# Kernel optimization log

Hardware: AMD Instinct MI355X
Metric: run time of the kernel (lower is better)

Reference implementation:

```python
import jax, jax.numpy as jnp
import numpy as np

B, CIN, COUT = 8, 16, 16
N_IN, N_OUT, E = 16384, 16384, 300000
FILTER_DIMS = [2, 16, 16, 16, 16, 16, CIN * COUT]  # spatial_dim -> filter_seq -> cin*cout


def setup_inputs() -> dict:
    key = jax.random.key(0)
    ks = jax.random.split(key, 12)
    points_in = jax.random.uniform(ks[0], (N_IN, 2), dtype=jnp.float32)
    points_out = jax.random.uniform(ks[1], (N_OUT, 2), dtype=jnp.float32)
    weights = jax.random.uniform(ks[2], (N_IN,), dtype=jnp.float32)  # quadrature weights
    features = jax.random.normal(ks[3], (B, CIN, N_IN), dtype=jnp.float32)
    idx_out = jnp.sort(jax.random.randint(ks[4], (E,), 0, N_OUT))
    idx_in = jax.random.randint(ks[5], (E,), 0, N_IN)
    eval_indices = jnp.stack([idx_out, idx_in], axis=1).astype(jnp.int32)
    inp = dict(points_in=points_in, points_out=points_out, weights=weights,
               features=features, eval_indices=eval_indices)
    for i in range(6):
        fan_in = FILTER_DIMS[i]
        inp[f"W{i}"] = (jax.random.normal(ks[6 + i], (FILTER_DIMS[i], FILTER_DIMS[i + 1]),
                                          dtype=jnp.float32) / np.float32(np.sqrt(fan_in)))
    return inp


def reference(points_in, points_out, weights, features, eval_indices, W0, W1, W2, W3, W4, W5):
    idx_out = eval_indices[:, 0]
    idx_in = eval_indices[:, 1]
    # eval_locs: [E, spatial_dim]
    locs = points_out[idx_out] - points_in[idx_in]
    # filter MLP with Sin activations, no bias (filter_mode='single')
    h = locs
    for W in (W0, W1, W2, W3, W4):
        h = jnp.sin(h @ W)
    filt = (h @ W5).reshape(-1, CIN, COUT)  # [E, cin, cout]
    w_e = weights[idx_in]                    # [E]
    feat_e = features[:, :, idx_in]          # [B, cin, E]
    # torch.einsum('n,nij,bin->bjn') -> per-edge values, laid out [E, B, cout] for segment_sum
    vals = jnp.einsum('e,eio,bie->ebo', w_e, filt, feat_e)
    integral = jax.ops.segment_sum(vals, idx_out, num_segments=N_OUT)  # [N_out, B, cout]
    return jnp.transpose(integral, (1, 2, 0))  # [B, cout, N_out]
```

## Files before the change

### kernel.cpp

```cpp
#include <hip/hip_runtime.h>

#define N_IN   16384
#define N_OUT  16384
#define NE     300000
#define SEGS   8
#define NWIN   (N_OUT / SEGS)
#define GRID_G 768
#define BKG    136
#define BSTR   544
#define SROW   256
#define NCHK   9375

#define MLPB   586
#define TRB    1024
#define SETB   80

typedef unsigned int   u32;
typedef unsigned short u16;
typedef __attribute__((ext_vector_type(4))) float f32x4;
typedef __attribute__((ext_vector_type(8))) short bf16x8;

__device__ __forceinline__ u16 f2bf(float x) {
    union { float f; u32 u; } v; v.f = x;
    u32 r = v.u + 0x7fffu + ((v.u >> 16) & 1u);
    return (u16)(r >> 16);
}

__device__ __forceinline__ float fast_sin(float t) {
    float r;
    asm("v_sin_f32 %0, %1" : "=v"(r) : "v"(t * 0.15915494309189535f));
    return r;
}

__global__ __launch_bounds__(256) void k_front(
        const float* __restrict__ pin, const float* __restrict__ pout,
        const float* __restrict__ wts, const int* __restrict__ ei,
        const float* __restrict__ W0, const float* __restrict__ W1,
        const float* __restrict__ W2, const float* __restrict__ W3,
        const float* __restrict__ W4, const float* __restrict__ W5,
        const float* __restrict__ feat,
        u16* __restrict__ ftb, u16* __restrict__ hB,
        int* __restrict__ segoff, u16* __restrict__ Bfrag) {
    __shared__ float tile[32][33];
    int tid = threadIdx.x, bid = blockIdx.x;

    if (bid < MLPB) {
        int e0 = (bid * 256 + tid) * 2;
        if (e0 >= NE) return;
        int4 q = *(const int4*)(ei + e0 * 2);
        float2 po0 = ((const float2*)pout)[q.x];
        float2 pi0 = ((const float2*)pin)[q.y];
        float2 po1 = ((const float2*)pout)[q.z];
        float2 pi1 = ((const float2*)pin)[q.w];
        float x0 = po0.x - pi0.x, y0 = po0.y - pi0.y;
        float x1 = po1.x - pi1.x, y1 = po1.y - pi1.y;

        float h0[16], h1[16];
#pragma unroll
        for (int j = 0; j < 16; ++j) {
            float wa = W0[j], wb = W0[16 + j];
            h0[j] = fast_sin(x0 * wa + y0 * wb);
            h1[j] = fast_sin(x1 * wa + y1 * wb);
        }
#pragma unroll
        for (int L = 0; L < 4; ++L) {
            const float* W = (L == 0) ? W1 : (L == 1) ? W2 : (L == 2) ? W3 : W4;
            float n0[16], n1[16];
#pragma unroll
            for (int j = 0; j < 16; ++j) {
                float a0 = 0.f, a1 = 0.f;
#pragma unroll
                for (int i = 0; i < 16; ++i) {
                    float w = W[i * 16 + j];
                    a0 = fmaf(h0[i], w, a0);
                    a1 = fmaf(h1[i], w, a1);
                }
                n0[j] = fast_sin(a0); n1[j] = fast_sin(a1);
            }
#pragma unroll
            for (int j = 0; j < 16; ++j) { h0[j] = n0[j]; h1[j] = n1[j]; }
        }
        float we0 = wts[q.y], we1 = wts[q.w];
        u16* hp = hB + ((size_t)(e0 >> 5)) * 512 + (e0 & 31);
#pragma unroll
        for (int j = 0; j < 16; ++j) {
            u32 pk = (u32)f2bf(we0 * h0[j]) | ((u32)f2bf(we1 * h1[j]) << 16);
            *(u32*)(hp + j * 32) = pk;
        }
    } else if (bid < MLPB + TRB) {
        int jb = (bid - MLPB) * 2;
        int tx = tid & 31, ty = tid >> 5;
#pragma unroll
        for (int t = 0; t < 2; ++t) {
            int job = jb + t;
            int n0 = (job & 511) * 32, c0 = (job >> 9) * 32;
#pragma unroll
            for (int k = 0; k < 4; ++k)
                tile[ty + k * 8][tx] = feat[(size_t)(c0 + ty + k * 8) * N_IN + n0 + tx];
            __syncthreads();
#pragma unroll
            for (int k = 0; k < 4; ++k)
                ftb[(size_t)(n0 + ty + k * 8) * 128 + c0 + tx] = f2bf(tile[tx][ty + k * 8]);
            __syncthreads();
        }
    } else {
        int g = (bid - MLPB - TRB) * 256 + tid;
        if (g <= N_OUT) {
            if (g == N_OUT) segoff[g] = NE;
            else {
                int lo = 0, hi = NE;
                while (lo < hi) { int m = (lo + hi) >> 1; if (ei[2 * m] < g) lo = m + 1; else hi = m; }
                segoff[g] = lo;
            }
        }
        if (g < 4096) {
            int ks = g >> 9, rem = g & 511, l = rem >> 3, e = rem & 7;
            int k = ks * 32 + ((l >> 4) << 3) + e;
            int o = l & 15;
            Bfrag[g] = f2bf(W5[(k >> 4) * 256 + ((k & 15) << 4) + o]);
        }
    }
}

#define EIW(IA, IB, BSE) do {                                             \
    int g_ = (BSE) + 2 * pr; g_ = g_ <= NE - 2 ? g_ : NE - 2;             \
    int4 q_ = *(const int4*)(ei + 2 * g_); IA = q_.y; IB = q_.w; } while (0)

#define FTW(FA, FB, IA, IB) do {                                          \
    FA = ftb4[(size_t)(u32)(IA) * 16 + oct];                              \
    FB = ftb4[(size_t)(u32)(IB) * 16 + oct]; } while (0)

#define BQW(BQ, BSE) do {                                                 \
    int ch_ = (BSE) >> 5; ch_ = ch_ <= NCHK - 1 ? ch_ : NCHK - 1;         \
    BQ = *(const bf16x8*)(hB + (size_t)ch_ * 512 + (j << 5) + (kg << 3)); } while (0)

#define STGW(DST, FA, FB) do {                                            \
    u32 aw_[4] = {FA.x, FA.y, FA.z, FA.w};                                \
    u32 bw_[4] = {FB.x, FB.y, FB.z, FB.w};                                \
    int wb_ = bloc * BSTR + (pr >> 2) * BKG + 2 * (pr & 3);               \
    _Pragma("unroll")                                                     \
    for (int m_ = 0; m_ < 8; ++m_) {                                      \
        u32 lo_ = (m_ & 1) ? (aw_[m_ >> 1] >> 16) : (aw_[m_ >> 1] & 0xffffu);      \
        u32 hi_ = (m_ & 1) ? (bw_[m_ >> 1] & 0xffff0000u) : (bw_[m_ >> 1] << 16);  \
        *(u32*)&(DST)[wb_ + (ibase + m_) * 8] = lo_ | hi_;                \
    } } while (0)

#define PIECE(KLO, KHI) do {                                              \
    if ((KLO) == 0 && (KHI) == 32) {                                      \
        acc0 = __builtin_amdgcn_mfma_f32_16x16x32_bf16(a0, bqC, acc0, 0, 0, 0); \
        acc1 = __builtin_amdgcn_mfma_f32_16x16x32_bf16(a1, bqC, acc1, 0, 0, 0); \
    } else {                                                              \
        bf16x8 bm_;                                                       \
        _Pragma("unroll")                                                 \
        for (int e_ = 0; e_ < 8; ++e_) {                                  \
            int k_ = kg * 8 + e_;                                         \
            bm_[e_] = (k_ >= (KLO) && k_ < (KHI)) ? bqC[e_] : (short)0;   \
        }                                                                 \
        acc0 = __builtin_amdgcn_mfma_f32_16x16x32_bf16(a0, bm_, acc0, 0, 0, 0); \
        acc1 = __builtin_amdgcn_mfma_f32_16x16x32_bf16(a1, bm_, acc1, 0, 0, 0); \
    } } while (0)

#define DUMP(SS) do {                                                     \
    u32 l0_ = (u32)f2bf(acc0[0]) | ((u32)f2bf(acc0[1]) << 16);            \
    u32 l1_ = (u32)f2bf(acc0[2]) | ((u32)f2bf(acc0[3]) << 16);            \
    *(uint2*)&S_lds[(b0 * SEGS + (SS)) * SROW + j * 16 + kg * 4] = make_uint2(l0_, l1_); \
    u32 l2_ = (u32)f2bf(acc1[0]) | ((u32)f2bf(acc1[1]) << 16);            \
    u32 l3_ = (u32)f2bf(acc1[2]) | ((u32)f2bf(acc1[3]) << 16);            \
    *(uint2*)&S_lds[((b0 + 1) * SEGS + (SS)) * SROW + j * 16 + kg * 4] = make_uint2(l2_, l3_); \
    acc0 = (f32x4){0.f, 0.f, 0.f, 0.f}; acc1 = (f32x4){0.f, 0.f, 0.f, 0.f}; \
} while (0)

#define SEG1(ST, EN, SS) do {                                             \
    int klo_ = (ST) > base_ ? (ST) - base_ : 0;                           \
    int khi_ = (EN) < ce_ ? (EN) - base_ : 32;                            \
    if (khi_ > klo_) PIECE(klo_, khi_);                                   \
    if ((EN) <= ce_ && (EN) > lb_) DUMP(SS);                              \
} while (0)

#define SEGALL() do {                                                     \
    SEG1(sA, sB, 0); SEG1(sB, sC, 1); SEG1(sC, sD, 2); SEG1(sD, sE, 3);   \
    SEG1(sE, sF, 4); SEG1(sF, sG, 5); SEG1(sG, sH, 6); SEG1(sH, sI, 7);   \
} while (0)

#define ITER(C, FA_S, FB_S) do {                                          \
    int base_ = base0 + 32 * (C); int ce_ = base_ + 32;                   \
    int lb_ = (C) ? base_ : base_ - 1;                                    \
    u16* rb_ = stW + ((C) & 1) * 1088;                                    \
    bf16x8 a0 = *(const bf16x8*)&rb_[(lane >> 4) * BKG + (lane & 15) * 8]; \
    bf16x8 a1 = *(const bf16x8*)&rb_[BSTR + (lane >> 4) * BKG + (lane & 15) * 8]; \
    STGW(stW + (((C) & 1) ^ 1) * 1088, FA_S, FB_S);                       \
    FTW(FA_S, FB_S, eiA, eiB);                                            \
    EIW(eiA2, eiB2, base_ + 128);                                         \
    bf16x8 bqT; BQW(bqT, base_ + 96);                                     \
    SEGALL();                                                             \
    bqC = bqN; bqN = bqL; bqL = bqT; eiA = eiA2; eiB = eiB2;              \
} while (0)

__global__ __launch_bounds__(256, 3) void k_gather(
        const int* __restrict__ ei, const u16* __restrict__ ftb,
        const u16* __restrict__ hB, const int* __restrict__ segoff,
        const u16* __restrict__ Bfrag, float* __restrict__ out)
{
    __shared__ __align__(16) u16 stA[4 * 2 * 2 * BSTR];
    __shared__ __align__(16) u16 S_lds[8 * SEGS * SROW];

    int tid = threadIdx.x, lane = tid & 63, wave = tid >> 6;
    int b0 = wave * 2;
    int pr = lane >> 2, c4 = lane & 3;
    int bloc = c4 >> 1, ibase = (c4 & 1) * 8;
    int oct = b0 * 2 + c4;
    int j = lane & 15, kg = lane >> 4;
    u16* stW = stA + wave * (2 * 2 * BSTR);
    const uint4* ftb4 = (const uint4*)ftb;

    bf16x8 bfr[8];
#pragma unroll
    for (int ks = 0; ks < 8; ++ks)
        bfr[ks] = *(const bf16x8*)(Bfrag + ks * 512 + lane * 8);

    for (int w = blockIdx.x; w < NWIN; w += GRID_G) {
        int s0 = w * SEGS;
        const int* so = segoff + s0;
        int sA = so[0], sB = so[1], sC = so[2], sD = so[3], sE = so[4];
        int sF = so[5], sG = so[6], sH = so[7], sI = so[8];

        int e0 = sA, e1 = sI;
        int base0 = e0 & ~31;
        int nc = (e1 - base0 + 31) >> 5;

        f32x4 acc0 = {0.f, 0.f, 0.f, 0.f}, acc1 = {0.f, 0.f, 0.f, 0.f};

        if (nc > 0) {
            int eiA, eiB, eiA2, eiB2;
            uint4 fa0, fb0, fa1, fb1;
            bf16x8 bqC, bqN, bqL;
            EIW(eiA, eiB, base0);        FTW(fa0, fb0, eiA, eiB);
            BQW(bqC, base0);
            EIW(eiA, eiB, base0 + 32);   FTW(fa1, fb1, eiA, eiB);
            BQW(bqN, base0 + 32);
            STGW(stW, fa0, fb0);
            EIW(eiA, eiB, base0 + 64);   FTW(fa0, fb0, eiA, eiB);
            BQW(bqL, base0 + 64);
            EIW(eiA, eiB, base0 + 96);

            for (int c = 0; c < nc; c += 2) {
                ITER(c, fa1, fb1);
                if (c + 1 < nc) ITER(c + 1, fa0, fb0);
            }
        } else {
            u32* zz = (u32*)&S_lds[b0 * SEGS * SROW];
            for (int I = lane; I < SEGS * SROW / 2; I += 64) zz[I] = 0;
        }

#pragma unroll
        for (int bb = 0; bb < 2; ++bb) {
            int b = b0 + bb;
            f32x4 ap = {0.f, 0.f, 0.f, 0.f};
#pragma unroll
            for (int ks = 0; ks < 8; ++ks) {
                bf16x8 af = *(const bf16x8*)
                    &S_lds[(b * SEGS + (lane & 7)) * SROW + ks * 32 + kg * 8];
                ap = __builtin_amdgcn_mfma_f32_16x16x32_bf16(af, bfr[ks], ap, 0, 0, 0);
            }
            int o = lane & 15;
            if (kg < 2)
                *(float4*)(out + (((size_t)(b * 16 + o)) << 14) + s0 + kg * 4) =
                    make_float4(ap[0], ap[1], ap[2], ap[3]);
        }
    }
}

extern "C" void kernel_launch(void* const* d_in, const int* in_sizes, int n_in,
                              void* d_out, int out_size, void* d_ws, size_t ws_size,
                              hipStream_t stream) {
    const float* pin  = (const float*)d_in[0];
    const float* pout = (const float*)d_in[1];
    const float* wts  = (const float*)d_in[2];
    const float* feat = (const float*)d_in[3];
    const int*   ei   = (const int*)d_in[4];
    const float* W0   = (const float*)d_in[5];
    const float* W1   = (const float*)d_in[6];
    const float* W2   = (const float*)d_in[7];
    const float* W3   = (const float*)d_in[8];
    const float* W4   = (const float*)d_in[9];
    const float* W5   = (const float*)d_in[10];
    float* out = (float*)d_out;

    u16* ftb    = (u16*)d_ws;
    u16* hB     = ftb + (size_t)N_IN * 128;
    int* segoff = (int*)(hB + (size_t)NCHK * 512 + 64);
    u16* Bfrag  = (u16*)(segoff + 16388);

    k_front<<<MLPB + TRB + SETB, 256, 0, stream>>>(
        pin, pout, wts, ei, W0, W1, W2, W3, W4, W5, feat,
        ftb, hB, segoff, Bfrag);
    k_gather<<<GRID_G, 256, 0, stream>>>(ei, ftb, hB, segoff, Bfrag, out);
}
```

Baseline: 55.91 us.

## Swizzle segment LDS tile, merge batch epilogue into one MFMA, single-buffer staging

The per-segment partial-sum tile in LDS now uses an XOR-style swizzled row layout, which should reduce bank conflicts on both the DUMP writes and the epilogue reads. The epilogue now packs two batches times eight segments into the 16 rows of one MFMA chain instead of running two half-empty chains, so every lane stores output. The per-wave edge staging buffer goes from double to single buffering, relying on in-order LDS access within a wave, which halves that LDS footprint. The risk is that single buffering serialises reads and writes to the staging area and may add waits.

```diff
diff --git a/kernel.cpp b/kernel.cpp
--- a/kernel.cpp
+++ b/kernel.cpp
@@ -134,7 +134,7 @@
     int ch_ = (BSE) >> 5; ch_ = ch_ <= NCHK - 1 ? ch_ : NCHK - 1;         \
     BQ = *(const bf16x8*)(hB + (size_t)ch_ * 512 + (j << 5) + (kg << 3)); } while (0)
 
-#define STGW(DST, FA, FB) do {                                            \
+#define STGW(FA, FB) do {                                                 \
     u32 aw_[4] = {FA.x, FA.y, FA.z, FA.w};                                \
     u32 bw_[4] = {FB.x, FB.y, FB.z, FB.w};                                \
     int wb_ = bloc * BSTR + (pr >> 2) * BKG + 2 * (pr & 3);               \
@@ -142,7 +142,7 @@
     for (int m_ = 0; m_ < 8; ++m_) {                                      \
         u32 lo_ = (m_ & 1) ? (aw_[m_ >> 1] >> 16) : (aw_[m_ >> 1] & 0xffffu);      \
         u32 hi_ = (m_ & 1) ? (bw_[m_ >> 1] & 0xffff0000u) : (bw_[m_ >> 1] << 16);  \
-        *(u32*)&(DST)[wb_ + (ibase + m_) * 8] = lo_ | hi_;                \
+        *(u32*)&stW[wb_ + (ibase + m_) * 8] = lo_ | hi_;                  \
     } } while (0)
 
 #define PIECE(KLO, KHI) do {                                              \
@@ -161,12 +161,17 @@
     } } while (0)
 
 #define DUMP(SS) do {                                                     \
+    int c_ = j * 2 + (kg >> 1);                                           \
+    int r0_ = b0 * SEGS + (SS);                                           \
+    int r1_ = r0_ + SEGS;                                                 \
     u32 l0_ = (u32)f2bf(acc0[0]) | ((u32)f2bf(acc0[1]) << 16);            \
     u32 l1_ = (u32)f2bf(acc0[2]) | ((u32)f2bf(acc0[3]) << 16);            \
-    *(uint2*)&S_lds[(b0 * SEGS + (SS)) * SROW + j * 16 + kg * 4] = make_uint2(l0_, l1_); \
+    *(uint2*)&S_lds[r0_ * 256 + (((c_ + r0_) & 31) << 3) + ((kg & 1) << 2)] = \
+        make_uint2(l0_, l1_);                                             \
     u32 l2_ = (u32)f2bf(acc1[0]) | ((u32)f2bf(acc1[1]) << 16);            \
     u32 l3_ = (u32)f2bf(acc1[2]) | ((u32)f2bf(acc1[3]) << 16);            \
-    *(uint2*)&S_lds[((b0 + 1) * SEGS + (SS)) * SROW + j * 16 + kg * 4] = make_uint2(l2_, l3_); \
+    *(uint2*)&S_lds[r1_ * 256 + (((c_ + r1_) & 31) << 3) + ((kg & 1) << 2)] = \
+        make_uint2(l2_, l3_);                                             \
     acc0 = (f32x4){0.f, 0.f, 0.f, 0.f}; acc1 = (f32x4){0.f, 0.f, 0.f, 0.f}; \
 } while (0)
 
@@ -185,10 +190,9 @@
 #define ITER(C, FA_S, FB_S) do {                                          \
     int base_ = base0 + 32 * (C); int ce_ = base_ + 32;                   \
     int lb_ = (C) ? base_ : base_ - 1;                                    \
-    u16* rb_ = stW + ((C) & 1) * 1088;                                    \
-    bf16x8 a0 = *(const bf16x8*)&rb_[(lane >> 4) * BKG + (lane & 15) * 8]; \
-    bf16x8 a1 = *(const bf16x8*)&rb_[BSTR + (lane >> 4) * BKG + (lane & 15) * 8]; \
-    STGW(stW + (((C) & 1) ^ 1) * 1088, FA_S, FB_S);                       \
+    bf16x8 a0 = *(const bf16x8*)&stW[(lane >> 4) * BKG + (lane & 15) * 8]; \
+    bf16x8 a1 = *(const bf16x8*)&stW[BSTR + (lane >> 4) * BKG + (lane & 15) * 8]; \
+    STGW(FA_S, FB_S);                          \
     FTW(FA_S, FB_S, eiA, eiB);                                            \
     EIW(eiA2, eiB2, base_ + 128);                                         \
     bf16x8 bqT; BQW(bqT, base_ + 96);                                     \
@@ -201,7 +205,7 @@
         const u16* __restrict__ hB, const int* __restrict__ segoff,
         const u16* __restrict__ Bfrag, float* __restrict__ out)
 {
-    __shared__ __align__(16) u16 stA[4 * 2 * 2 * BSTR];
+    __shared__ __align__(16) u16 stA[4 * 2 * BSTR];
     __shared__ __align__(16) u16 S_lds[8 * SEGS * SROW];
 
     int tid = threadIdx.x, lane = tid & 63, wave = tid >> 6;
@@ -210,7 +214,7 @@
     int bloc = c4 >> 1, ibase = (c4 & 1) * 8;
     int oct = b0 * 2 + c4;
     int j = lane & 15, kg = lane >> 4;
-    u16* stW = stA + wave * (2 * 2 * BSTR);
+    u16* stW = stA + wave * (2 * BSTR);
     const uint4* ftb4 = (const uint4*)ftb;
 
     bf16x8 bfr[8];
@@ -238,7 +242,7 @@
             BQW(bqC, base0);
             EIW(eiA, eiB, base0 + 32);   FTW(fa1, fb1, eiA, eiB);
             BQW(bqN, base0 + 32);
-            STGW(stW, fa0, fb0);
+            STGW(fa0, fb0);
             EIW(eiA, eiB, base0 + 64);   FTW(fa0, fb0, eiA, eiB);
             BQW(bqL, base0 + 64);
             EIW(eiA, eiB, base0 + 96);
@@ -248,24 +252,23 @@
                 if (c + 1 < nc) ITER(c + 1, fa0, fb0);
             }
         } else {
-            u32* zz = (u32*)&S_lds[b0 * SEGS * SROW];
-            for (int I = lane; I < SEGS * SROW / 2; I += 64) zz[I] = 0;
-        }
-
-#pragma unroll
-        for (int bb = 0; bb < 2; ++bb) {
-            int b = b0 + bb;
+            u32* zz = (u32*)&S_lds[wave * 4096];
+            for (int I = lane; I < 2048; I += 64) zz[I] = 0;
+        }
+
+        {
+            int r = wave * 16 + (lane & 15);
             f32x4 ap = {0.f, 0.f, 0.f, 0.f};
 #pragma unroll
             for (int ks = 0; ks < 8; ++ks) {
                 bf16x8 af = *(const bf16x8*)
-                    &S_lds[(b * SEGS + (lane & 7)) * SROW + ks * 32 + kg * 8];
+                    &S_lds[r * 256 + (((ks * 4 + kg + r) & 31) << 3)];
                 ap = __builtin_amdgcn_mfma_f32_16x16x32_bf16(af, bfr[ks], ap, 0, 0, 0);
             }
             int o = lane & 15;
-            if (kg < 2)
-                *(float4*)(out + (((size_t)(b * 16 + o)) << 14) + s0 + kg * 4) =
-                    make_float4(ap[0], ap[1], ap[2], ap[3]);
+            int b = b0 + (kg >> 1);
+            *(float4*)(out + (((size_t)(b * 16 + o)) << 14) + s0 + ((kg & 1) << 2)) =
+                make_float4(ap[0], ap[1], ap[2], ap[3]);
         }
     }
 }
```

After: 53.65 us (median of 2 runs). 4.0% less time.
